# Kernel optimization log

Hardware: AMD Instinct MI355X
Metric: run time of the kernel (lower is better)

The kernel has to match this reference:

```python
import jax, jax.numpy as jnp
import numpy as np

L, C, K, V, G, T, NC, CIN = 9, 256, 3, 25, 9, 128, 60, 3


def _ln(x, w, b, axes, eps=1e-5):
    # LayerNorm over (channels, joints) per time step, affine params broadcast over time
    m = x.mean(axes, keepdims=True)
    v = x.var(axes, keepdims=True)
    return (x - m) * jax.lax.rsqrt(v + eps) * w + b


def setup_inputs() -> dict:
    key = jax.random.key(0)
    ks = jax.random.split(key, 8)
    s = 0.02  # weight init scale
    return {
        "x": jax.random.normal(ks[0], (1, CIN, T, V), jnp.float32),
        "A": jax.random.uniform(ks[1], (K, V, V), jnp.float32),
        "ln_in_w": jnp.ones((CIN, V), jnp.float32),
        "ln_in_b": jnp.zeros((CIN, V), jnp.float32),
        "W_in": jax.random.normal(ks[2], (C, CIN), jnp.float32) * s,
        "b_in": jnp.zeros((C,), jnp.float32),
        "Wg": jax.random.normal(ks[3], (L, K * C, C), jnp.float32) * s,
        "bg": jnp.zeros((L, K * C), jnp.float32),
        "ln1_w": jnp.ones((L, C, V), jnp.float32),
        "ln1_b": jnp.zeros((L, C, V), jnp.float32),
        "Wt": jax.random.normal(ks[4], (L, C, C, G), jnp.float32) * s,
        "bt": jnp.zeros((L, C), jnp.float32),
        "ln2_w": jnp.ones((L, C, V), jnp.float32),
        "ln2_b": jnp.zeros((L, C, V), jnp.float32),
        "imp": jnp.ones((L, K, V, V), jnp.float32),
        "W_out": jax.random.normal(ks[5], (NC, C), jnp.float32) * s,
        "b_out": jnp.zeros((NC,), jnp.float32),
    }


def reference(x, A, ln_in_w, ln_in_b, W_in, b_in, Wg, bg, ln1_w, ln1_b,
              Wt, bt, ln2_w, ln2_b, imp, W_out, b_out):
    ghalf = G // 2
    Al = A[None] * imp                      # (L, K, V, V) edge-importance weighted adjacency
    xs = x[0].transpose(1, 0, 2)            # (T, CIN, V): stream frames
    fifo0 = jnp.zeros((L, C, G, V), x.dtype)

    def step(carry, xt):
        fifo, fifo_res = carry
        # input LayerNorm + 1x1 conv (fcn_in)
        h = _ln(xt, ln_in_w, ln_in_b, (0, 1))
        h = jnp.einsum('oc,cv->ov', W_in, h) + b_in[:, None]   # (C, V)
        new_f, new_fr = [], []
        for l in range(L):
            res = h                                             # identity residual (in==out, stride==1)
            # graph conv: 1x1 conv -> (K, C, V), einsum with partitioned adjacency
            y = (jnp.einsum('oc,cv->ov', Wg[l], h) + bg[l][:, None]).reshape(K, C, V)
            z = jnp.einsum('kcv,kvw->cw', y, Al[l])             # (C, V)
            # FIFO shift: newest frame at time index 0
            f = jnp.concatenate([z[:, None, :], fifo[l, :, :-1]], axis=1)      # (C, G, V)
            fr = jnp.concatenate([res[:, None, :], fifo_res[l, :, :-1]], axis=1)
            # tcn: LN -> ReLU -> temporal conv (G,1) -> LN
            a = jax.nn.relu(_ln(f, ln1_w[l][:, None, :], ln1_b[l][:, None, :], (0, 2)))
            t = jnp.einsum('ocg,cgv->ov', Wt[l], a) + bt[l][:, None]           # (C, V)
            t = _ln(t, ln2_w[l], ln2_b[l], (0, 1))
            # residual from center of residual FIFO, then ReLU
            h = jax.nn.relu(t + fr[:, ghalf])
            new_f.append(f)
            new_fr.append(fr)
        pooled = h.mean(axis=1)                                 # avg_pool2d over (T=1, V)
        logits = W_out @ pooled + b_out                         # (NC,)
        return (jnp.stack(new_f), jnp.stack(new_fr)), logits

    _, out = jax.lax.scan(step, (fifo0, fifo0), xs)
    return out  # (T, NC): per-frame class logits
```

## Files before the change

### kernel.cpp

```cpp
#include <hip/hip_runtime.h>

#define TT  128
#define CC  256
#define VV  25
#define KK  3
#define GG  9
#define LL  9
#define NCC 60
#define CINN 3
#define TV    (TT*VV)
#define N4    4096
#define KDIM2 (CC*GG)
#define UR    ((TT+8)*32)

typedef __attribute__((ext_vector_type(8))) short bf16x8;
typedef __attribute__((ext_vector_type(4))) float f32x4;
typedef unsigned short us16;

__device__ __forceinline__ us16 f2bf(float f) {
    union { float f; unsigned u; } a; a.f = f;
    unsigned r = a.u + 0x7fff + ((a.u >> 16) & 1);
    return (us16)(r >> 16);
}
__device__ __forceinline__ bf16x8 ld8(const us16* p) { return *(const bf16x8*)p; }


__global__ void k_cvt(const float* __restrict__ src, us16* __restrict__ dst, int n) {
    int i = blockIdx.x * 256 + threadIdx.x;
    if (i < n) dst[i] = f2bf(src[i]);
}

__global__ void k_wtt(const float* __restrict__ Wt, us16* __restrict__ Wt2b) {
    int i = blockIdx.x * 256 + threadIdx.x;
    if (i >= LL*CC*CC*GG) return;
    int kk = i % (CC*GG);
    int o  = (i / (CC*GG)) % CC;
    int l  = i / (CC*CC*GG);
    int g = kk >> 8, c = kk & 255;
    Wt2b[i] = f2bf(Wt[((size_t)(l*CC + o)*CC + c)*GG + g]);
}

__global__ void k_alt(const float* __restrict__ A, const float* __restrict__ imp,
                      us16* __restrict__ AlTb) {
    int i = blockIdx.x * 256 + threadIdx.x;
    if (i >= LL*KK*32*32) return;
    int v = i & 31, w = (i >> 5) & 31;
    int lk = i >> 10, k = lk % KK, l = lk / KK;
    float val = 0.f;
    if (v < VV && w < VV)
        val = A[(k*VV+v)*VV + w] * imp[((size_t)(l*KK+k)*VV+v)*VV + w];
    AlTb[i] = f2bf(val);
}

__global__ void k_bgal(const float* __restrict__ A, const float* __restrict__ imp,
                       const float* __restrict__ bg, float* __restrict__ bgAl) {
    int i = blockIdx.x * 256 + threadIdx.x;
    if (i >= LL*CC*32) return;
    int w = i & 31, c = (i >> 5) & 255, l = i >> 13;
    float s = 0.f;
    if (w < VV) {
        for (int k = 0; k < KK; k++) {
            float col = 0.f;
            for (int v = 0; v < VV; v++)
                col += A[(k*VV+v)*VV + w] * imp[((size_t)(l*KK+k)*VV+v)*VV + w];
            s += bg[l*KK*CC + k*CC + c] * col;
        }
    }
    bgAl[i] = s;
}


__global__ __launch_bounds__(256) void k_h0(const float* __restrict__ x,
                                            const float* __restrict__ lnw,
                                            const float* __restrict__ lnb,
                                            const float* __restrict__ Win,
                                            const float* __restrict__ bin,
                                            float* __restrict__ H,
                                            us16* __restrict__ Hbt2) {
    int t = blockIdx.x, tid = threadIdx.x;
    __shared__ float sx[CINN*VV];
    __shared__ float sh[CINN*VV];
    if (tid < CINN*VV)
        sx[tid] = x[(size_t)(tid/VV)*TV + t*VV + (tid%VV)];
    __syncthreads();
    float s = 0.f, q = 0.f;
    for (int i = 0; i < CINN*VV; i++) { float v = sx[i]; s += v; q += v*v; }
    float m  = s * (1.f/75.f);
    float var = q * (1.f/75.f) - m*m;
    float rs = rsqrtf(var + 1e-5f);
    if (tid < CINN*VV)
        sh[tid] = (sx[tid]-m)*rs*lnw[tid] + lnb[tid];
    __syncthreads();
    int c = tid;
    float w0 = Win[c*3+0], w1 = Win[c*3+1], w2 = Win[c*3+2], b = bin[c];
    #pragma unroll
    for (int v = 0; v < VV; v++) {
        float acc = b + w0*sh[v] + w1*sh[VV+v] + w2*sh[2*VV+v];
        H[(size_t)c*N4 + t*32 + v] = acc;
        Hbt2[(size_t)(t*32 + v)*CC + c] = f2bf(acc);
    }
    #pragma unroll
    for (int v = VV; v < 32; v++)
        Hbt2[(size_t)(t*32 + v)*CC + c] = 0;
}


__device__ __forceinline__ void blk_reduce2(float& s, float& q, float* red) {
    #pragma unroll
    for (int off = 32; off; off >>= 1) {
        s += __shfl_down(s, off);
        q += __shfl_down(q, off);
    }
    int lane = threadIdx.x & 63, w = threadIdx.x >> 6;
    if (lane == 0) { red[w] = s; red[4+w] = q; }
    __syncthreads();
    s = red[0]+red[1]+red[2]+red[3];
    q = red[4]+red[5]+red[6]+red[7];
}


__global__ __launch_bounds__(256) void k_gemm1(const us16* __restrict__ A,
                                               const us16* __restrict__ Bt,
                                               us16* __restrict__ Ybt) {
    const int tid = threadIdx.x;
    const int wave = tid >> 6, lane = tid & 63, quad = lane >> 4, l16 = lane & 15;
    const int m0w = blockIdx.y * 64 + (wave & 1) * 32;
    const int n0w = blockIdx.x * 64 + (wave >> 1) * 32;
    const us16* ap = A + (size_t)(m0w + l16) * CC + quad * 8;
    const us16* bp = Bt + (size_t)(n0w + l16) * CC + quad * 8;
    f32x4 acc[2][2] = {};
    #pragma unroll
    for (int s = 0; s < 8; s++) {
        bf16x8 a0 = ld8(ap + s*32);
        bf16x8 a1 = ld8(ap + s*32 + 16*CC);
        bf16x8 b0 = ld8(bp + s*32);
        bf16x8 b1 = ld8(bp + s*32 + 16*CC);
        acc[0][0] = __builtin_amdgcn_mfma_f32_16x16x32_bf16(a0, b0, acc[0][0], 0,0,0);
        acc[0][1] = __builtin_amdgcn_mfma_f32_16x16x32_bf16(a0, b1, acc[0][1], 0,0,0);
        acc[1][0] = __builtin_amdgcn_mfma_f32_16x16x32_bf16(a1, b0, acc[1][0], 0,0,0);
        acc[1][1] = __builtin_amdgcn_mfma_f32_16x16x32_bf16(a1, b1, acc[1][1], 0,0,0);
    }
    #pragma unroll
    for (int mt = 0; mt < 2; mt++)
        #pragma unroll
        for (int nt = 0; nt < 2; nt++)
            #pragma unroll
            for (int r = 0; r < 4; r++) {
                int m = m0w + mt*16 + quad*4 + r;
                int n = n0w + nt*16 + l16;
                int k = m >> 8, c = m & 255;
                int t = n >> 5, v = n & 31;
                Ybt[((size_t)(t*CC + c))*96 + k*32 + v] = f2bf(acc[mt][nt][r]);
            }
}


__global__ __launch_bounds__(256) void k_adj(const us16* __restrict__ Ybt,
                                             const us16* __restrict__ AlTb,
                                             const float* __restrict__ bgAl,
                                             const float* __restrict__ lnw,
                                             const float* __restrict__ lnb,
                                             us16* __restrict__ Ut2) {
    int t = blockIdx.x, tid = threadIdx.x;
    if (t >= TT) {
        int tp = t - TT, c = tid;
        #pragma unroll
        for (int w = 0; w < 32; w++) {
            float u = (w < VV) ? fmaxf(lnb[c*VV + w], 0.f) : 0.f;
            Ut2[(size_t)(tp*32 + w)*CC + c] = f2bf(u);
        }
        return;
    }
    __shared__ float red[8];
    const int wave = tid >> 6, lane = tid & 63, quad = lane >> 4, l16 = lane & 15;
    bf16x8 al[2][3];
    #pragma unroll
    for (int nt = 0; nt < 2; nt++)
        #pragma unroll
        for (int s = 0; s < 3; s++)
            al[nt][s] = ld8(AlTb + (size_t)(s*32 + nt*16 + l16)*32 + quad*8);
    f32x4 z[4][2];
    #pragma unroll
    for (int mt = 0; mt < 4; mt++) { z[mt][0] = (f32x4){}; z[mt][1] = (f32x4){}; }
    #pragma unroll
    for (int mt = 0; mt < 4; mt++) {
        const us16* yp = Ybt + ((size_t)(t*CC + wave*64 + mt*16 + l16))*96 + quad*8;
        #pragma unroll
        for (int s = 0; s < 3; s++) {
            bf16x8 a = ld8(yp + s*32);
            z[mt][0] = __builtin_amdgcn_mfma_f32_16x16x32_bf16(a, al[0][s], z[mt][0], 0,0,0);
            z[mt][1] = __builtin_amdgcn_mfma_f32_16x16x32_bf16(a, al[1][s], z[mt][1], 0,0,0);
        }
    }
    float s_ = 0.f, q_ = 0.f;
    #pragma unroll
    for (int mt = 0; mt < 4; mt++)
        #pragma unroll
        for (int nt = 0; nt < 2; nt++)
            #pragma unroll
            for (int r = 0; r < 4; r++) {
                int c = wave*64 + mt*16 + quad*4 + r;
                int w = nt*16 + l16;
                float zb = z[mt][nt][r] + bgAl[c*32 + w];
                z[mt][nt][r] = zb;
                if (w < VV) { s_ += zb; q_ += zb*zb; }
            }
    blk_reduce2(s_, q_, red);
    float m = s_ * (1.f/6400.f);
    float var = q_ * (1.f/6400.f) - m*m;
    float rs = rsqrtf(var + 1e-5f);
    #pragma unroll
    for (int mt = 0; mt < 4; mt++)
        #pragma unroll
        for (int nt = 0; nt < 2; nt++) {
            int w = nt*16 + l16;
            if (w < VV) {
                int c0 = wave*64 + mt*16 + quad*4;
                ushort4 pk;
                float u0 = fmaxf((z[mt][nt][0]-m)*rs*lnw[(c0+0)*VV+w] + lnb[(c0+0)*VV+w], 0.f);
                float u1 = fmaxf((z[mt][nt][1]-m)*rs*lnw[(c0+1)*VV+w] + lnb[(c0+1)*VV+w], 0.f);
                float u2 = fmaxf((z[mt][nt][2]-m)*rs*lnw[(c0+2)*VV+w] + lnb[(c0+2)*VV+w], 0.f);
                float u3 = fmaxf((z[mt][nt][3]-m)*rs*lnw[(c0+3)*VV+w] + lnb[(c0+3)*VV+w], 0.f);
                pk.x = f2bf(u0); pk.y = f2bf(u1); pk.z = f2bf(u2); pk.w = f2bf(u3);
                *(ushort4*)(Ut2 + (size_t)((t+8)*32 + w)*CC + c0) = pk;
            }
        }
    #pragma unroll
    for (int r = VV; r < 32; r++)
        Ut2[(size_t)((t+8)*32 + r)*CC + tid] = 0;
}


__global__ __launch_bounds__(256) void k_gemm2(const us16* __restrict__ A,
                                               const us16* __restrict__ Ut2,
                                               float* __restrict__ TC) {
    const int tid = threadIdx.x;
    const int wave = tid >> 6, lane = tid & 63, quad = lane >> 4, l16 = lane & 15;
    const int m0w = blockIdx.y * 64 + (wave & 1) * 32;
    const int n0w = blockIdx.x * 64 + (wave >> 1) * 32;
    const us16* ap = A + (size_t)(m0w + l16) * KDIM2 + quad * 8;
    f32x4 acc00 = {}, acc01 = {}, acc10 = {}, acc11 = {};
    bf16x8 a0, a1, b0, b1;

    auto loadAB = [&](int k0, bf16x8& x0, bf16x8& x1, bf16x8& y0, bf16x8& y1) {
        x0 = ld8(ap + k0);
        x1 = ld8(ap + k0 + 16*KDIM2);
        int g = k0 >> 8;
        const us16* bp = Ut2 + (size_t)(n0w + (8-g)*32 + l16)*CC + (k0 & 255) + quad*8;
        y0 = ld8(bp);
        y1 = ld8(bp + 16*CC);
    };
    loadAB(0, a0, a1, b0, b1);
    #pragma unroll 4
    for (int k0 = 32; k0 < KDIM2; k0 += 32) {
        bf16x8 c0, c1, d0, d1;
        loadAB(k0, c0, c1, d0, d1);
        acc00 = __builtin_amdgcn_mfma_f32_16x16x32_bf16(a0, b0, acc00, 0,0,0);
        acc01 = __builtin_amdgcn_mfma_f32_16x16x32_bf16(a0, b1, acc01, 0,0,0);
        acc10 = __builtin_amdgcn_mfma_f32_16x16x32_bf16(a1, b0, acc10, 0,0,0);
        acc11 = __builtin_amdgcn_mfma_f32_16x16x32_bf16(a1, b1, acc11, 0,0,0);
        a0 = c0; a1 = c1; b0 = d0; b1 = d1;
    }
    acc00 = __builtin_amdgcn_mfma_f32_16x16x32_bf16(a0, b0, acc00, 0,0,0);
    acc01 = __builtin_amdgcn_mfma_f32_16x16x32_bf16(a0, b1, acc01, 0,0,0);
    acc10 = __builtin_amdgcn_mfma_f32_16x16x32_bf16(a1, b0, acc10, 0,0,0);
    acc11 = __builtin_amdgcn_mfma_f32_16x16x32_bf16(a1, b1, acc11, 0,0,0);

    const int r0 = m0w + quad*4;
    const int col = n0w + l16;
    #pragma unroll
    for (int r = 0; r < 4; r++) {
        TC[(size_t)(r0 + r)*N4 + col]           = acc00[r];
        TC[(size_t)(r0 + r)*N4 + col + 16]      = acc01[r];
        TC[(size_t)(r0 + 16 + r)*N4 + col]      = acc10[r];
        TC[(size_t)(r0 + 16 + r)*N4 + col + 16] = acc11[r];
    }
}


__global__ __launch_bounds__(256) void k_ln2(const float* __restrict__ TC,
                                             const float* __restrict__ bt,
                                             const float* __restrict__ lnw,
                                             const float* __restrict__ lnb,
                                             const float* __restrict__ Hin,
                                             float* __restrict__ Hout,
                                             us16* __restrict__ Hbt2) {
    int t = blockIdx.x, tid = threadIdx.x;
    __shared__ float sv[CC*33];
    __shared__ float red[8];
    #pragma unroll
    for (int j = 0; j < 8; j++) {
        int c = j*32 + (tid >> 3);
        int v4 = (tid & 7) * 4;
        float4 x = *(const float4*)(TC + (size_t)c*N4 + t*32 + v4);
        sv[c*33 + v4+0] = x.x; sv[c*33 + v4+1] = x.y;
        sv[c*33 + v4+2] = x.z; sv[c*33 + v4+3] = x.w;
    }
    __syncthreads();
    int c = tid;
    float btc = bt[c];
    float vals[VV];
    float s = 0.f, q = 0.f;
    #pragma unroll
    for (int v = 0; v < VV; v++) {
        float x = sv[c*33 + v] + btc;
        vals[v] = x; s += x; q += x*x;
    }
    blk_reduce2(s, q, red);
    float m = s * (1.f/6400.f);
    float var = q * (1.f/6400.f) - m*m;
    float rs = rsqrtf(var + 1e-5f);
    __syncthreads();
    #pragma unroll
    for (int v = 0; v < VV; v++) {
        float res = (t >= 4) ? Hin[(size_t)c*N4 + (t-4)*32 + v] : 0.f;
        float o = fmaxf((vals[v]-m)*rs*lnw[c*VV+v] + lnb[c*VV+v] + res, 0.f);
        Hout[(size_t)c*N4 + t*32 + v] = o;
        sv[c*33 + v] = o;
    }
    __syncthreads();
    #pragma unroll
    for (int v = 0; v < VV; v++)
        Hbt2[(size_t)(t*32 + v)*CC + tid] = f2bf(sv[tid*33 + v]);
    #pragma unroll
    for (int v = VV; v < 32; v++)
        Hbt2[(size_t)(t*32 + v)*CC + tid] = 0;
}


__global__ __launch_bounds__(256) void k_out(const float* __restrict__ H,
                                             const float* __restrict__ Wout,
                                             const float* __restrict__ bout,
                                             float* __restrict__ out) {
    int t = blockIdx.x, tid = threadIdx.x;
    __shared__ float sp[CC];
    float s = 0.f;
    for (int v = 0; v < VV; v++) s += H[(size_t)tid*N4 + t*32 + v];
    sp[tid] = s * (1.f/VV);
    __syncthreads();
    if (tid < NCC) {
        float acc = bout[tid];
        for (int c = 0; c < CC; c++) acc = fmaf(Wout[tid*CC+c], sp[c], acc);
        out[t*NCC + tid] = acc;
    }
}


extern "C" void kernel_launch(void* const* d_in, const int* in_sizes, int n_in,
                              void* d_out, int out_size, void* d_ws, size_t ws_size,
                              hipStream_t stream) {
    const float* x    = (const float*)d_in[0];
    const float* A    = (const float*)d_in[1];
    const float* lniw = (const float*)d_in[2];
    const float* lnib = (const float*)d_in[3];
    const float* Win  = (const float*)d_in[4];
    const float* bin  = (const float*)d_in[5];
    const float* Wg   = (const float*)d_in[6];
    const float* bg   = (const float*)d_in[7];
    const float* ln1w = (const float*)d_in[8];
    const float* ln1b = (const float*)d_in[9];
    const float* Wt   = (const float*)d_in[10];
    const float* bt   = (const float*)d_in[11];
    const float* ln2w = (const float*)d_in[12];
    const float* ln2b = (const float*)d_in[13];
    const float* imp  = (const float*)d_in[14];
    const float* Wout = (const float*)d_in[15];
    const float* bout = (const float*)d_in[16];
    float* out = (float*)d_out;

    float* ws = (float*)d_ws;
    size_t off = 0;
    auto alloc = [&](size_t n) { float* p = ws + off; off += (n + 255) & ~(size_t)255; return p; };
    float* H0   = alloc((size_t)CC*N4);
    float* H1   = alloc((size_t)CC*N4);
    float* TC   = alloc((size_t)CC*N4);
    float* bgAl = alloc((size_t)LL*CC*32);
    us16* Wgb  = (us16*)alloc((size_t)LL*KK*CC*CC/2);
    us16* Wt2b = (us16*)alloc((size_t)LL*CC*KDIM2/2);
    us16* Hbt2 = (us16*)alloc((size_t)N4*CC/2);
    us16* Ut2  = (us16*)alloc((size_t)UR*CC/2);
    us16* AlTb = (us16*)alloc((size_t)LL*KK*32*32/2);
    us16* Ybt  = (us16*)alloc((size_t)TT*CC*96/2);
    (void)ws_size; (void)in_sizes; (void)n_in; (void)out_size;

    k_cvt<<<((LL*KK*CC*CC) + 255)/256, 256, 0, stream>>>(Wg, Wgb, LL*KK*CC*CC);
    k_wtt<<<((LL*CC*CC*GG) + 255)/256, 256, 0, stream>>>(Wt, Wt2b);
    k_alt<<<((LL*KK*32*32) + 255)/256, 256, 0, stream>>>(A, imp, AlTb);
    k_bgal<<<((LL*CC*32) + 255)/256, 256, 0, stream>>>(A, imp, bg, bgAl);
    k_h0<<<TT, 256, 0, stream>>>(x, lniw, lnib, Win, bin, H0, Hbt2);

    float* Hin = H0; float* Hout = H1;
    for (int l = 0; l < LL; l++) {
        k_gemm1<<<dim3(N4/64, (KK*CC)/64), 256, 0, stream>>>(
            Wgb + (size_t)l*KK*CC*CC, Hbt2, Ybt);
        k_adj<<<TT + 8, 256, 0, stream>>>(
            Ybt, AlTb + (size_t)l*KK*32*32, bgAl + (size_t)l*CC*32,
            ln1w + l*CC*VV, ln1b + l*CC*VV, Ut2);
        k_gemm2<<<dim3(N4/64, CC/64), 256, 0, stream>>>(
            Wt2b + (size_t)l*CC*KDIM2, Ut2, TC);
        k_ln2<<<TT, 256, 0, stream>>>(
            TC, bt + l*CC, ln2w + l*CC*VV, ln2b + l*CC*VV, Hin, Hout, Hbt2);
        float* tmp = Hin; Hin = Hout; Hout = tmp;
    }
    k_out<<<TT, 256, 0, stream>>>(Hin, Wout, bout, out);
}
```

Before: 867.2 us.

## Split-K temporal GEMM, stage gemm1 epilogue in LDS, fuse prep kernels

```diff
diff --git a/kernel.cpp b/kernel.cpp
--- a/kernel.cpp
+++ b/kernel.cpp
@@ -12,6 +12,8 @@
 #define N4    4096
 #define KDIM2 (CC*GG)
 #define UR    ((TT+8)*32)
+#define KSPLIT 4
+#define KCH   (KDIM2/KSPLIT)
 
 typedef __attribute__((ext_vector_type(8))) short bf16x8;
 typedef __attribute__((ext_vector_type(4))) float f32x4;
@@ -25,48 +27,49 @@
 __device__ __forceinline__ bf16x8 ld8(const us16* p) { return *(const bf16x8*)p; }
 
 
-__global__ void k_cvt(const float* __restrict__ src, us16* __restrict__ dst, int n) {
+#define PN1 (LL*KK*CC*CC)
+#define PN2 (LL*CC*CC*GG)
+#define PN3 (LL*KK*32*32)
+#define PN4 (LL*CC*32)
+#define PTOT (PN1+PN2+PN3+PN4)
+
+__global__ void k_prep(const float* __restrict__ Wg, const float* __restrict__ Wt,
+                       const float* __restrict__ A, const float* __restrict__ imp,
+                       const float* __restrict__ bg,
+                       us16* __restrict__ Wgb, us16* __restrict__ Wt2b,
+                       us16* __restrict__ AlTb, float* __restrict__ bgAl) {
     int i = blockIdx.x * 256 + threadIdx.x;
-    if (i < n) dst[i] = f2bf(src[i]);
-}
-
-__global__ void k_wtt(const float* __restrict__ Wt, us16* __restrict__ Wt2b) {
-    int i = blockIdx.x * 256 + threadIdx.x;
-    if (i >= LL*CC*CC*GG) return;
-    int kk = i % (CC*GG);
-    int o  = (i / (CC*GG)) % CC;
-    int l  = i / (CC*CC*GG);
-    int g = kk >> 8, c = kk & 255;
-    Wt2b[i] = f2bf(Wt[((size_t)(l*CC + o)*CC + c)*GG + g]);
-}
-
-__global__ void k_alt(const float* __restrict__ A, const float* __restrict__ imp,
-                      us16* __restrict__ AlTb) {
-    int i = blockIdx.x * 256 + threadIdx.x;
-    if (i >= LL*KK*32*32) return;
-    int v = i & 31, w = (i >> 5) & 31;
-    int lk = i >> 10, k = lk % KK, l = lk / KK;
-    float val = 0.f;
-    if (v < VV && w < VV)
-        val = A[(k*VV+v)*VV + w] * imp[((size_t)(l*KK+k)*VV+v)*VV + w];
-    AlTb[i] = f2bf(val);
-}
-
-__global__ void k_bgal(const float* __restrict__ A, const float* __restrict__ imp,
-                       const float* __restrict__ bg, float* __restrict__ bgAl) {
-    int i = blockIdx.x * 256 + threadIdx.x;
-    if (i >= LL*CC*32) return;
-    int w = i & 31, c = (i >> 5) & 255, l = i >> 13;
-    float s = 0.f;
-    if (w < VV) {
-        for (int k = 0; k < KK; k++) {
-            float col = 0.f;
-            for (int v = 0; v < VV; v++)
-                col += A[(k*VV+v)*VV + w] * imp[((size_t)(l*KK+k)*VV+v)*VV + w];
-            s += bg[l*KK*CC + k*CC + c] * col;
+    if (i < PN1) {
+        Wgb[i] = f2bf(Wg[i]);
+    } else if (i < PN1 + PN2) {
+        int j = i - PN1;
+        int kk = j % (CC*GG);
+        int o  = (j / (CC*GG)) % CC;
+        int l  = j / (CC*CC*GG);
+        int g = kk >> 8, c = kk & 255;
+        Wt2b[j] = f2bf(Wt[((size_t)(l*CC + o)*CC + c)*GG + g]);
+    } else if (i < PN1 + PN2 + PN3) {
+        int j = i - PN1 - PN2;
+        int v = j & 31, w = (j >> 5) & 31;
+        int lk = j >> 10, k = lk % KK, l = lk / KK;
+        float val = 0.f;
+        if (v < VV && w < VV)
+            val = A[(k*VV+v)*VV + w] * imp[((size_t)(l*KK+k)*VV+v)*VV + w];
+        AlTb[j] = f2bf(val);
+    } else if (i < PTOT) {
+        int j = i - PN1 - PN2 - PN3;
+        int w = j & 31, c = (j >> 5) & 255, l = j >> 13;
+        float s = 0.f;
+        if (w < VV) {
+            for (int k = 0; k < KK; k++) {
+                float col = 0.f;
+                for (int v = 0; v < VV; v++)
+                    col += A[(k*VV+v)*VV + w] * imp[((size_t)(l*KK+k)*VV+v)*VV + w];
+                s += bg[l*KK*CC + k*CC + c] * col;
+            }
         }
-    }
-    bgAl[i] = s;
+        bgAl[j] = s;
+    }
 }
 
 
@@ -122,6 +125,7 @@
 __global__ __launch_bounds__(256) void k_gemm1(const us16* __restrict__ A,
                                                const us16* __restrict__ Bt,
                                                us16* __restrict__ Ybt) {
+    __shared__ us16 Yl[64*72];
     const int tid = threadIdx.x;
     const int wave = tid >> 6, lane = tid & 63, quad = lane >> 4, l16 = lane & 15;
     const int m0w = blockIdx.y * 64 + (wave & 1) * 32;
@@ -146,12 +150,22 @@
         for (int nt = 0; nt < 2; nt++)
             #pragma unroll
             for (int r = 0; r < 4; r++) {
-                int m = m0w + mt*16 + quad*4 + r;
-                int n = n0w + nt*16 + l16;
-                int k = m >> 8, c = m & 255;
-                int t = n >> 5, v = n & 31;
-                Ybt[((size_t)(t*CC + c))*96 + k*32 + v] = f2bf(acc[mt][nt][r]);
+                int m_loc = (wave & 1)*32 + mt*16 + quad*4 + r;
+                int n_loc = (wave >> 1)*32 + nt*16 + l16;
+                Yl[m_loc*72 + n_loc] = f2bf(acc[mt][nt][r]);
             }
+    __syncthreads();
+    const int kidx = (blockIdx.y * 64) >> 8;
+    const int c0   = (blockIdx.y * 64) & 255;
+    const int t0   = blockIdx.x * 2;
+    #pragma unroll
+    for (int u = 0; u < 2; u++) {
+        int q = tid*2 + u;
+        int ch = q & 3, row = q >> 2;
+        int cl = row & 63, tl = row >> 6;
+        bf16x8 val = *(const bf16x8*)(Yl + cl*72 + tl*32 + ch*8);
+        *(bf16x8*)(Ybt + ((size_t)((t0+tl)*CC + c0 + cl))*96 + kidx*32 + ch*8) = val;
+    }
 }
 
 
@@ -233,11 +247,14 @@
 
 __global__ __launch_bounds__(256) void k_gemm2(const us16* __restrict__ A,
                                                const us16* __restrict__ Ut2,
-                                               float* __restrict__ TC) {
+                                               float* __restrict__ TCp) {
     const int tid = threadIdx.x;
     const int wave = tid >> 6, lane = tid & 63, quad = lane >> 4, l16 = lane & 15;
     const int m0w = blockIdx.y * 64 + (wave & 1) * 32;
     const int n0w = blockIdx.x * 64 + (wave >> 1) * 32;
+    const int ks = blockIdx.z;
+    const int kbeg = ks * KCH, kend = kbeg + KCH;
+    float* TC = TCp + (size_t)ks * CC * N4;
     const us16* ap = A + (size_t)(m0w + l16) * KDIM2 + quad * 8;
     f32x4 acc00 = {}, acc01 = {}, acc10 = {}, acc11 = {};
     bf16x8 a0, a1, b0, b1;
@@ -250,9 +267,9 @@
         y0 = ld8(bp);
         y1 = ld8(bp + 16*CC);
     };
-    loadAB(0, a0, a1, b0, b1);
-    #pragma unroll 4
-    for (int k0 = 32; k0 < KDIM2; k0 += 32) {
+    loadAB(kbeg, a0, a1, b0, b1);
+    #pragma unroll 3
+    for (int k0 = kbeg + 32; k0 < kend; k0 += 32) {
         bf16x8 c0, c1, d0, d1;
         loadAB(k0, c0, c1, d0, d1);
         acc00 = __builtin_amdgcn_mfma_f32_16x16x32_bf16(a0, b0, acc00, 0,0,0);
@@ -278,7 +295,7 @@
 }
 
 
-__global__ __launch_bounds__(256) void k_ln2(const float* __restrict__ TC,
+__global__ __launch_bounds__(256) void k_ln2(const float* __restrict__ TCp,
                                              const float* __restrict__ bt,
                                              const float* __restrict__ lnw,
                                              const float* __restrict__ lnb,
@@ -292,7 +309,13 @@
     for (int j = 0; j < 8; j++) {
         int c = j*32 + (tid >> 3);
         int v4 = (tid & 7) * 4;
-        float4 x = *(const float4*)(TC + (size_t)c*N4 + t*32 + v4);
+        size_t base = (size_t)c*N4 + t*32 + v4;
+        float4 x = *(const float4*)(TCp + base);
+        #pragma unroll
+        for (int s = 1; s < KSPLIT; s++) {
+            float4 y = *(const float4*)(TCp + (size_t)s*CC*N4 + base);
+            x.x += y.x; x.y += y.y; x.z += y.z; x.w += y.w;
+        }
         sv[c*33 + v4+0] = x.x; sv[c*33 + v4+1] = x.y;
         sv[c*33 + v4+2] = x.z; sv[c*33 + v4+3] = x.w;
     }
@@ -310,7 +333,6 @@
     float m = s * (1.f/6400.f);
     float var = q * (1.f/6400.f) - m*m;
     float rs = rsqrtf(var + 1e-5f);
-    __syncthreads();
     #pragma unroll
     for (int v = 0; v < VV; v++) {
         float res = (t >= 4) ? Hin[(size_t)c*N4 + (t-4)*32 + v] : 0.f;
@@ -318,7 +340,6 @@
         Hout[(size_t)c*N4 + t*32 + v] = o;
         sv[c*33 + v] = o;
     }
-    __syncthreads();
     #pragma unroll
     for (int v = 0; v < VV; v++)
         Hbt2[(size_t)(t*32 + v)*CC + tid] = f2bf(sv[tid*33 + v]);
@@ -373,7 +394,7 @@
     auto alloc = [&](size_t n) { float* p = ws + off; off += (n + 255) & ~(size_t)255; return p; };
     float* H0   = alloc((size_t)CC*N4);
     float* H1   = alloc((size_t)CC*N4);
-    float* TC   = alloc((size_t)CC*N4);
+    float* TCp  = alloc((size_t)KSPLIT*CC*N4);
     float* bgAl = alloc((size_t)LL*CC*32);
     us16* Wgb  = (us16*)alloc((size_t)LL*KK*CC*CC/2);
     us16* Wt2b = (us16*)alloc((size_t)LL*CC*KDIM2/2);
@@ -383,10 +404,8 @@
     us16* Ybt  = (us16*)alloc((size_t)TT*CC*96/2);
     (void)ws_size; (void)in_sizes; (void)n_in; (void)out_size;
 
-    k_cvt<<<((LL*KK*CC*CC) + 255)/256, 256, 0, stream>>>(Wg, Wgb, LL*KK*CC*CC);
-    k_wtt<<<((LL*CC*CC*GG) + 255)/256, 256, 0, stream>>>(Wt, Wt2b);
-    k_alt<<<((LL*KK*32*32) + 255)/256, 256, 0, stream>>>(A, imp, AlTb);
-    k_bgal<<<((LL*CC*32) + 255)/256, 256, 0, stream>>>(A, imp, bg, bgAl);
+    k_prep<<<(PTOT + 255)/256, 256, 0, stream>>>(Wg, Wt, A, imp, bg,
+                                                 Wgb, Wt2b, AlTb, bgAl);
     k_h0<<<TT, 256, 0, stream>>>(x, lniw, lnib, Win, bin, H0, Hbt2);
 
     float* Hin = H0; float* Hout = H1;
@@ -396,10 +415,10 @@
         k_adj<<<TT + 8, 256, 0, stream>>>(
             Ybt, AlTb + (size_t)l*KK*32*32, bgAl + (size_t)l*CC*32,
             ln1w + l*CC*VV, ln1b + l*CC*VV, Ut2);
-        k_gemm2<<<dim3(N4/64, CC/64), 256, 0, stream>>>(
-            Wt2b + (size_t)l*CC*KDIM2, Ut2, TC);
+        k_gemm2<<<dim3(N4/64, CC/64, KSPLIT), 256, 0, stream>>>(
+            Wt2b + (size_t)l*CC*KDIM2, Ut2, TCp);
         k_ln2<<<TT, 256, 0, stream>>>(
-            TC, bt + l*CC, ln2w + l*CC*VV, ln2b + l*CC*VV, Hin, Hout, Hbt2);
+            TCp, bt + l*CC, ln2w + l*CC*VV, ln2b + l*CC*VV, Hin, Hout, Hbt2);
         float* tmp = Hin; Hin = Hout; Hout = tmp;
     }
     k_out<<<TT, 256, 0, stream>>>(Hin, Wout, bout, out);
```

After: 880.2 us. About the same (+1.5%).
